# Kernel tuning notes

Hardware: AMD Instinct MI355X
Metric: run time of the kernel (lower is better)

Reference implementation:

```python
import jax, jax.numpy as jnp
import numpy as np

DILATIONS = [2 ** i for i in range(9)] * 3  # 27 layers
RD, SD, QD = 32, 512, 256


def conv1d(x, w, b, dilation=1, padding=0):
    # x: [B,C,T], w: [O,I,K], b: [O]
    out = jax.lax.conv_general_dilated(
        x, w, window_strides=(1,), padding=[(padding, padding)],
        rhs_dilation=(dilation,), dimension_numbers=('NCH', 'OIH', 'NCH'))
    return out + b[None, :, None]


def setup_inputs() -> dict:
    key = jax.random.key(0)
    ks = jax.random.split(key, 16)
    T = 131072
    L = len(DILATIONS)
    s = 0.05
    inp = {
        'x': jax.random.normal(ks[0], (1, 1, T), dtype=jnp.float32),
        'Wc': jax.random.normal(ks[1], (RD, 1, 3), dtype=jnp.float32) * s,
        'bc': jnp.zeros((RD,), dtype=jnp.float32),
        'Wt': jax.random.normal(ks[2], (L, RD, RD, 3), dtype=jnp.float32) * s,
        'bt': jnp.zeros((L, RD), dtype=jnp.float32),
        'Ws': jax.random.normal(ks[3], (L, RD, RD, 3), dtype=jnp.float32) * s,
        'bs': jnp.zeros((L, RD), dtype=jnp.float32),
        'Wskip': jax.random.normal(ks[4], (L, SD, RD, 1), dtype=jnp.float32) * s,
        'bskip': jnp.zeros((L, SD), dtype=jnp.float32),
        'Wdense': jax.random.normal(ks[5], (L, RD, RD, 1), dtype=jnp.float32) * s,
        'bdense': jnp.zeros((L, RD), dtype=jnp.float32),
        'Wp1': jax.random.normal(ks[6], (SD, SD, 1), dtype=jnp.float32) * s,
        'bp1': jnp.zeros((SD,), dtype=jnp.float32),
        'Wp2': jax.random.normal(ks[7], (QD, SD, 1), dtype=jnp.float32) * s,
        'bp2': jnp.zeros((QD,), dtype=jnp.float32),
    }
    return inp


def reference(x, Wc, bc, Wt, bt, Ws, bs, Wskip, bskip, Wdense, bdense, Wp1, bp1, Wp2, bp2):
    # causal conv: kernel 3, padding 1 (same length)
    x = conv1d(x, Wc, bc, dilation=1, padding=1)  # [1, RD, T]
    skip = jnp.zeros((1, SD, x.shape[2]), dtype=jnp.float32)
    for i, d in enumerate(DILATIONS):
        xin = x
        g = jnp.tanh(conv1d(x, Wt[i], bt[i], d, d)) * jax.nn.sigmoid(conv1d(x, Ws[i], bs[i], d, d))
        skip = skip + conv1d(g, Wskip[i], bskip[i])
        x = conv1d(g, Wdense[i], bdense[i]) + xin
    # NOTE: the original applies F.relu(x) on the residual path but then
    # overwrites x with the skip-path result, so that relu is dead code.
    out = conv1d(jax.nn.relu(conv1d(skip, Wp1, bp1)), Wp2, bp2)  # [1, QD, T]
    return jax.nn.log_softmax(out, axis=1)
```

## Files before the change

### kernel.cpp

```cpp
#include <hip/hip_runtime.h>

#define T_LEN 131072
#define RD 32
#define SD 512
#define QD 256
#define NL 27
#define KTOT (NL * RD)
#define GPAD 256

typedef __attribute__((ext_vector_type(8))) short short8;
typedef __attribute__((ext_vector_type(4))) float floatx4;

__device__ __forceinline__ unsigned short f2bf(float f) {
    union { float f; unsigned int i; } v; v.f = f;
    unsigned int r = v.i + 0x7fffu + ((v.i >> 16) & 1u);
    return (unsigned short)(r >> 16);
}

__device__ __forceinline__ void gload_lds16(const void* g, void* l) {
    __builtin_amdgcn_global_load_lds(
        (const __attribute__((address_space(1))) unsigned int*)g,
        (__attribute__((address_space(3))) unsigned int*)l, 16, 0, 0);
}

__global__ __launch_bounds__(256)
void k_conv_init(const float* __restrict__ x, const float* __restrict__ Wc,
                 const float* __restrict__ bc,
                 float* __restrict__ xaG, unsigned short* __restrict__ xabG,
                 float* __restrict__ xbG, unsigned short* __restrict__ xbbG)
{
    const int gid = blockIdx.x * 256 + threadIdx.x;

    if (gid < 4 * GPAD * RD) {
        const int region = gid >> 13;
        const int idx = gid & (GPAD * RD - 1);
        float* fg; unsigned short* hg;
        const size_t post = (size_t)(GPAD + T_LEN) * RD;
        switch (region) {
            case 0:  fg = xaG;        hg = xabG;        break;
            case 1:  fg = xaG + post; hg = xabG + post; break;
            case 2:  fg = xbG;        hg = xbbG;        break;
            default: fg = xbG + post; hg = xbbG + post; break;
        }
        fg[idx] = 0.f;
        hg[idx] = 0;
    }

    const int t = gid;
    const float xm = (t > 0) ? x[t - 1] : 0.f;
    const float x0 = x[t];
    const float xp = (t < T_LEN - 1) ? x[t + 1] : 0.f;
    float* row = xaG + (size_t)(GPAD + t) * RD;
    unsigned short* rowb = xabG + (size_t)(GPAD + t) * RD;
#pragma unroll
    for (int o = 0; o < RD; ++o) {
        const float v = bc[o] + Wc[o * 3 + 0] * xm + Wc[o * 3 + 1] * x0 + Wc[o * 3 + 2] * xp;
        row[o] = v;
        rowb[o] = f2bf(v);
    }
}

__global__ __launch_bounds__(256)
void k_wprep(const float* __restrict__ Wt, const float* __restrict__ Ws,
             const float* __restrict__ Wd,
             unsigned short* __restrict__ Wg, unsigned short* __restrict__ Wdb)
{
    const int idx = blockIdx.x * 256 + threadIdx.x;
    const int n1 = NL * 64 * 96;
    const int n2 = NL * RD * RD;
    if (idx < n1) {
        const int l = idx / (64 * 96);
        const int rem = idx % (64 * 96);
        const int m = rem / 96;
        const int k = rem % 96;
        const int j = k / 32;
        const int c = k % 32;
        float v;
        if (m < 32) v = Wt[(((size_t)l * RD + m) * RD + c) * 3 + j];
        else        v = Ws[(((size_t)l * RD + (m - 32)) * RD + c) * 3 + j];
        Wg[idx] = f2bf(v);
    } else if (idx < n1 + n2) {
        const int i2 = idx - n1;
        Wdb[i2] = f2bf(Wd[i2]);
    }
}

__global__ __launch_bounds__(256, 4)
void k_layer_stage(const float* __restrict__ xin,
                   const unsigned short* __restrict__ xinb,
                   float* __restrict__ xout,
                   unsigned short* __restrict__ xoutb,
                   unsigned short* __restrict__ Gt,
                   const unsigned short* __restrict__ Wg,
                   const unsigned short* __restrict__ Wdb,
                   const float* __restrict__ bt, const float* __restrict__ bs,
                   const float* __restrict__ bd, int d, int layer)
{
    __shared__ unsigned short bandsL[3][128 * 32];
    __shared__ unsigned short gtileL[128 * 32];

    const int tid = threadIdx.x;
    const int lane = tid & 63;
    const int w = tid >> 6;
    const int quad = lane >> 4;
    const int l16 = lane & 15;
    const int rbase = w * 32;
    const bool last = (layer == NL - 1);
    const floatx4 vzero = {0.f, 0.f, 0.f, 0.f};

    const int r16c = lane >> 2;
    const int scB = (lane & 3) ^ ((lane >> 3) & 3);
    const long long gbase = (long long)blockIdx.x * 128 + rbase;

#pragma unroll
    for (int j = 0; j < 3; ++j) {
        const long long b0 = gbase + (long long)(j - 1) * d;
#pragma unroll
        for (int i = 0; i < 2; ++i)
            gload_lds16(xinb + (b0 + i * 16 + r16c) * RD + scB * 8,
                        &bandsL[j][(rbase + i * 16) * 32]);
    }
    asm volatile("" ::: "memory");

    floatx4 xi[2][2];
    if (!last) {
#pragma unroll
        for (int nt = 0; nt < 2; ++nt) {
            const long long t = gbase + nt * 16 + l16;
#pragma unroll
            for (int mt = 0; mt < 2; ++mt)
                xi[nt][mt] = *reinterpret_cast<const floatx4*>(
                    xin + (size_t)t * RD + mt * 16 + quad * 4);
        }
    }
    asm volatile("s_waitcnt vmcnt(8)" ::: "memory");

    short8 afr[3][4];
#pragma unroll
    for (int j = 0; j < 3; ++j)
#pragma unroll
        for (int mt = 0; mt < 4; ++mt)
            afr[j][mt] = *reinterpret_cast<const short8*>(
                Wg + (size_t)(mt * 16 + l16) * 96 + j * 32 + quad * 8);

    floatx4 acc[4][2];
#pragma unroll
    for (int mt = 0; mt < 4; ++mt)
#pragma unroll
        for (int nt = 0; nt < 2; ++nt) acc[mt][nt] = vzero;

#pragma unroll
    for (int nt = 0; nt < 2; ++nt) {
        const int rloc = rbase + nt * 16 + l16;
        const int key2 = (rloc >> 1) & 3;
#pragma unroll
        for (int j = 0; j < 3; ++j) {
            const short8 bb = *reinterpret_cast<const short8*>(
                &bandsL[j][rloc * 32 + ((quad ^ key2) * 8)]);
#pragma unroll
            for (int mt = 0; mt < 4; ++mt)
                acc[mt][nt] = __builtin_amdgcn_mfma_f32_16x16x32_bf16(
                    afr[j][mt], bb, acc[mt][nt], 0, 0, 0);
        }
    }

#pragma unroll
    for (int nt = 0; nt < 2; ++nt) {
        const int rloc = rbase + nt * 16 + l16;
        const int key2 = (rloc >> 1) & 3;
        const long long t = (long long)blockIdx.x * 128 + rloc;
#pragma unroll
        for (int pair = 0; pair < 2; ++pair) {
            const floatx4 bt4 = *reinterpret_cast<const floatx4*>(bt + pair * 16 + quad * 4);
            const floatx4 bs4 = *reinterpret_cast<const floatx4*>(bs + pair * 16 + quad * 4);
            ushort4 u;
            unsigned short us[4];
#pragma unroll
            for (int r = 0; r < 4; ++r) {
                const float a1 = acc[pair][nt][r] + bt4[r];
                const float a2 = acc[2 + pair][nt][r] + bs4[r];
                const float th = 1.f - __fdividef(2.f, __expf(2.f * a1) + 1.f);
                const float sg = __fdividef(1.f, 1.f + __expf(-a2));
                us[r] = f2bf(th * sg);
            }
            u.x = us[0]; u.y = us[1]; u.z = us[2]; u.w = us[3];
            const int cbase = pair * 16 + quad * 4;
            if (!last) {
                const int colS = (pair * 2 + (quad >> 1)) ^ key2;
                *reinterpret_cast<ushort4*>(
                    &gtileL[rloc * 32 + colS * 8 + (quad & 1) * 4]) = u;
            }
            *reinterpret_cast<ushort4*>(
                Gt + ((size_t)layer * T_LEN + t) * RD + cbase) = u;
        }
    }

    if (!last) {
        short8 ad[2];
#pragma unroll
        for (int mt = 0; mt < 2; ++mt)
            ad[mt] = *reinterpret_cast<const short8*>(
                Wdb + (size_t)(mt * 16 + l16) * RD + quad * 8);

#pragma unroll
        for (int nt = 0; nt < 2; ++nt) {
            const int rloc = rbase + nt * 16 + l16;
            const int key2 = (rloc >> 1) & 3;
            const long long t = (long long)blockIdx.x * 128 + rloc;
            const short8 bg = *reinterpret_cast<const short8*>(
                &gtileL[rloc * 32 + ((quad ^ key2) * 8)]);
#pragma unroll
            for (int mt = 0; mt < 2; ++mt) {
                const floatx4 a2v = __builtin_amdgcn_mfma_f32_16x16x32_bf16(
                    ad[mt], bg, vzero, 0, 0, 0);
                const int m = mt * 16 + quad * 4;
                const floatx4 bd4 = *reinterpret_cast<const floatx4*>(bd + m);
                floatx4 o;
                ushort4 ob;
                o[0] = a2v[0] + bd4[0] + xi[nt][mt][0]; ob.x = f2bf(o[0]);
                o[1] = a2v[1] + bd4[1] + xi[nt][mt][1]; ob.y = f2bf(o[1]);
                o[2] = a2v[2] + bd4[2] + xi[nt][mt][2]; ob.z = f2bf(o[2]);
                o[3] = a2v[3] + bd4[3] + xi[nt][mt][3]; ob.w = f2bf(o[3]);
                *reinterpret_cast<floatx4*>(xout + (size_t)t * RD + m) = o;
                *reinterpret_cast<ushort4*>(xoutb + (size_t)t * RD + m) = ob;
            }
        }
    }
}

__global__ __launch_bounds__(256)
void k_wcomb(const float* __restrict__ Wp1, const float* __restrict__ Wskip,
             unsigned short* __restrict__ Wcomb)
{
    const int idx = blockIdx.x * 256 + threadIdx.x;
    if (idx >= SD * KTOT) return;
    const int m = idx / KTOT;
    const int k = idx % KTOT;
    const int l = k / RD;
    const int c = k % RD;
    const float* wp1r = Wp1 + (size_t)m * SD;
    const float* wsk = Wskip + (size_t)l * SD * RD + c;
    float acc = 0.f;
    for (int j = 0; j < SD; ++j) acc += wp1r[j] * wsk[(size_t)j * RD];
    Wcomb[((size_t)l * SD + m) * RD + c] = f2bf(acc);
}

__global__ __launch_bounds__(512)
void k_hbias(const float* __restrict__ Wp1, const float* __restrict__ bp1,
             const float* __restrict__ bskip, float* __restrict__ hbias)
{
    __shared__ float sb[SD];
    const int tid = threadIdx.x;
    float s = 0.f;
    for (int l = 0; l < NL; ++l) s += bskip[l * SD + tid];
    sb[tid] = s;
    __syncthreads();
    float acc = bp1[tid];
    const float* r = Wp1 + (size_t)tid * SD;
    for (int j = 0; j < SD; ++j) acc += r[j] * sb[j];
    hbias[tid] = acc;
}

__global__ __launch_bounds__(256)
void k_cvt(const float* __restrict__ src, unsigned short* __restrict__ dst, int n)
{
    const int i = blockIdx.x * 256 + threadIdx.x;
    if (i < n) dst[i] = f2bf(src[i]);
}

__global__ __launch_bounds__(256)
void k_gemm1(const unsigned short* __restrict__ A,
             const unsigned short* __restrict__ B,
             const float* __restrict__ hbias,
             unsigned short* __restrict__ ht)
{
    __shared__ unsigned short ldsA[2][128 * 32];
    __shared__ unsigned short ldsB[2][128 * 32];
    const int tid = threadIdx.x;
    const int lane = tid & 63;
    const int w = tid >> 6;
    const int wm = w & 1;
    const int wn = w >> 1;
    const int quad = lane >> 4;
    const int l16 = lane & 15;

    const int g = blockIdx.x;
    const int m0 = ((g >> 3) & 3) * 128;
    const int n0 = ((g & 7) + 8 * (g >> 5)) * 128;

    const int r4 = lane >> 2;
    const int c4 = lane & 3;
    const int srcc = c4 ^ ((r4 >> 1) & 3);
    const int swz = (l16 >> 1) & 3;

    floatx4 acc[4][4];
    const floatx4 vzero = {0.f, 0.f, 0.f, 0.f};
#pragma unroll
    for (int mt = 0; mt < 4; ++mt)
#pragma unroll
        for (int nt = 0; nt < 4; ++nt) acc[mt][nt] = vzero;

    const unsigned short* pA = A + (size_t)(m0 + r4) * RD + srcc * 8;
    const unsigned short* pB = B + (size_t)(n0 + r4) * RD + srcc * 8;

    for (int kc2 = 0; kc2 < 13; ++kc2) {
#pragma unroll
        for (int s = 0; s < 2; ++s) {
            const int kc = kc2 * 2 + s;
#pragma unroll
            for (int c = 0; c < 2; ++c) {
                const int row = w * 32 + c * 16;
                gload_lds16(pA + ((size_t)kc * SD + row) * RD, &ldsA[s][row * 32]);
                gload_lds16(pB + ((size_t)kc * T_LEN + row) * RD, &ldsB[s][row * 32]);
            }
        }
        __syncthreads();

#pragma unroll
        for (int s = 0; s < 2; ++s) {
            short8 afr[4], bfr[4];
#pragma unroll
            for (int mt = 0; mt < 4; ++mt)
                afr[mt] = *reinterpret_cast<const short8*>(
                    &ldsA[s][(wm * 64 + mt * 16 + l16) * 32 + (quad ^ swz) * 8]);
#pragma unroll
            for (int nt = 0; nt < 4; ++nt)
                bfr[nt] = *reinterpret_cast<const short8*>(
                    &ldsB[s][(wn * 64 + nt * 16 + l16) * 32 + (quad ^ swz) * 8]);
#pragma unroll
            for (int mt = 0; mt < 4; ++mt)
#pragma unroll
                for (int nt = 0; nt < 4; ++nt)
                    acc[mt][nt] = __builtin_amdgcn_mfma_f32_16x16x32_bf16(
                        afr[mt], bfr[nt], acc[mt][nt], 0, 0, 0);
        }
        __syncthreads();
    }
    {
        const int kc = 26;
#pragma unroll
        for (int c = 0; c < 2; ++c) {
            const int row = w * 32 + c * 16;
            gload_lds16(pA + ((size_t)kc * SD + row) * RD, &ldsA[0][row * 32]);
            gload_lds16(pB + ((size_t)kc * T_LEN + row) * RD, &ldsB[0][row * 32]);
        }
        __syncthreads();
        short8 afr[4], bfr[4];
#pragma unroll
        for (int mt = 0; mt < 4; ++mt)
            afr[mt] = *reinterpret_cast<const short8*>(
                &ldsA[0][(wm * 64 + mt * 16 + l16) * 32 + (quad ^ swz) * 8]);
#pragma unroll
        for (int nt = 0; nt < 4; ++nt)
            bfr[nt] = *reinterpret_cast<const short8*>(
                &ldsB[0][(wn * 64 + nt * 16 + l16) * 32 + (quad ^ swz) * 8]);
#pragma unroll
        for (int mt = 0; mt < 4; ++mt)
#pragma unroll
            for (int nt = 0; nt < 4; ++nt)
                acc[mt][nt] = __builtin_amdgcn_mfma_f32_16x16x32_bf16(
                    afr[mt], bfr[nt], acc[mt][nt], 0, 0, 0);
    }

#pragma unroll
    for (int mt = 0; mt < 4; ++mt) {
        const int m = m0 + wm * 64 + mt * 16 + quad * 4;
        const floatx4 hb = *reinterpret_cast<const floatx4*>(hbias + m);
        const size_t chunkbase = (size_t)(m >> 5) * T_LEN;
        const int mc = m & 31;
#pragma unroll
        for (int nt = 0; nt < 4; ++nt) {
            const int t = n0 + wn * 64 + nt * 16 + l16;
            ushort4 st;
            float v;
            v = acc[mt][nt][0] + hb[0]; st.x = f2bf(v > 0.f ? v : 0.f);
            v = acc[mt][nt][1] + hb[1]; st.y = f2bf(v > 0.f ? v : 0.f);
            v = acc[mt][nt][2] + hb[2]; st.z = f2bf(v > 0.f ? v : 0.f);
            v = acc[mt][nt][3] + hb[3]; st.w = f2bf(v > 0.f ? v : 0.f);
            *reinterpret_cast<ushort4*>(ht + (chunkbase + t) * RD + mc) = st;
        }
    }
}

__global__ __launch_bounds__(256)
void k_gemm2_lsm(const unsigned short* __restrict__ A,
                 const unsigned short* __restrict__ B,
                 const float* __restrict__ bp2,
                 float* __restrict__ out)
{
    __shared__ unsigned short ldsB[4][64 * 32];
    __shared__ float redmax[4 * 16 * 16];
    __shared__ float redsum[4 * 16 * 16];
    const int tid = threadIdx.x;
    const int lane = tid & 63;
    const int w = tid >> 6;
    const int quad = lane >> 4;
    const int l16 = lane & 15;
    const int m0 = w * 64;
    const int n0 = blockIdx.x * 64;

    const int r4 = lane >> 2;
    const int c4 = lane & 3;
    const int srcc = c4 ^ ((r4 >> 1) & 3);
    const int swz = (l16 >> 1) & 3;

    const unsigned short* ab[4];
#pragma unroll
    for (int mt = 0; mt < 4; ++mt)
        ab[mt] = A + (size_t)(m0 + mt * 16 + l16) * SD + quad * 8;

    const unsigned short* pB = B + (size_t)(n0 + w * 16 + r4) * RD + srcc * 8;

    floatx4 acc[4][4];
    const floatx4 vzero = {0.f, 0.f, 0.f, 0.f};
#pragma unroll
    for (int mt = 0; mt < 4; ++mt)
#pragma unroll
        for (int nt = 0; nt < 4; ++nt) acc[mt][nt] = vzero;

    for (int kc4 = 0; kc4 < 4; ++kc4) {
#pragma unroll
        for (int s = 0; s < 4; ++s)
            gload_lds16(pB + (size_t)(kc4 * 4 + s) * T_LEN * RD,
                        &ldsB[s][(w * 16) * 32]);
        __syncthreads();

#pragma unroll
        for (int s = 0; s < 4; ++s) {
            const int kc = kc4 * 4 + s;
            short8 afr[4];
#pragma unroll
            for (int mt = 0; mt < 4; ++mt)
                afr[mt] = *reinterpret_cast<const short8*>(ab[mt] + kc * 32);
            short8 bfr[4];
#pragma unroll
            for (int nt = 0; nt < 4; ++nt)
                bfr[nt] = *reinterpret_cast<const short8*>(
                    &ldsB[s][(nt * 16 + l16) * 32 + (quad ^ swz) * 8]);
#pragma unroll
            for (int mt = 0; mt < 4; ++mt)
#pragma unroll
                for (int nt = 0; nt < 4; ++nt)
                    acc[mt][nt] = __builtin_amdgcn_mfma_f32_16x16x32_bf16(
                        afr[mt], bfr[nt], acc[mt][nt], 0, 0, 0);
        }
        __syncthreads();
    }

#pragma unroll
    for (int mt = 0; mt < 4; ++mt) {
        const int mb = m0 + mt * 16 + quad * 4;
        const floatx4 bz = *reinterpret_cast<const floatx4*>(bp2 + mb);
#pragma unroll
        for (int nt = 0; nt < 4; ++nt)
#pragma unroll
            for (int j = 0; j < 4; ++j) acc[mt][nt][j] += bz[j];
    }

#pragma unroll
    for (int nt = 0; nt < 4; ++nt) {
        float lm = -1e30f;
#pragma unroll
        for (int mt = 0; mt < 4; ++mt)
#pragma unroll
            for (int j = 0; j < 4; ++j) lm = fmaxf(lm, acc[mt][nt][j]);
        redmax[nt * 256 + l16 * 16 + w * 4 + quad] = lm;
    }
    __syncthreads();

    float lse[4];
#pragma unroll
    for (int nt = 0; nt < 4; ++nt) {
        float gm = -1e30f;
#pragma unroll
        for (int i = 0; i < 16; ++i) gm = fmaxf(gm, redmax[nt * 256 + l16 * 16 + i]);
        float ls = 0.f;
#pragma unroll
        for (int mt = 0; mt < 4; ++mt)
#pragma unroll
            for (int j = 0; j < 4; ++j) ls += __expf(acc[mt][nt][j] - gm);
        redsum[nt * 256 + l16 * 16 + w * 4 + quad] = ls;
        lse[nt] = gm;
    }
    __syncthreads();

#pragma unroll
    for (int nt = 0; nt < 4; ++nt) {
        float tot = 0.f;
#pragma unroll
        for (int i = 0; i < 16; ++i) tot += redsum[nt * 256 + l16 * 16 + i];
        lse[nt] = lse[nt] + __logf(tot);
    }

#pragma unroll
    for (int mt = 0; mt < 4; ++mt) {
        const int mb = m0 + mt * 16 + quad * 4;
#pragma unroll
        for (int nt = 0; nt < 4; ++nt) {
            const int t = n0 + nt * 16 + l16;
#pragma unroll
            for (int j = 0; j < 4; ++j)
                out[(size_t)(mb + j) * T_LEN + t] = acc[mt][nt][j] - lse[nt];
        }
    }
}

extern "C" void kernel_launch(void* const* d_in, const int* in_sizes, int n_in,
                              void* d_out, int out_size, void* d_ws, size_t ws_size,
                              hipStream_t stream)
{
    (void)in_sizes; (void)n_in; (void)out_size; (void)ws_size;
    const float* x     = (const float*)d_in[0];
    const float* Wc    = (const float*)d_in[1];
    const float* bc    = (const float*)d_in[2];
    const float* Wt    = (const float*)d_in[3];
    const float* bt    = (const float*)d_in[4];
    const float* Ws    = (const float*)d_in[5];
    const float* bs    = (const float*)d_in[6];
    const float* Wskip = (const float*)d_in[7];
    const float* bskip = (const float*)d_in[8];
    const float* Wd    = (const float*)d_in[9];
    const float* bd    = (const float*)d_in[10];
    const float* Wp1   = (const float*)d_in[11];
    const float* bp1   = (const float*)d_in[12];
    const float* Wp2   = (const float*)d_in[13];
    const float* bp2   = (const float*)d_in[14];
    float* out = (float*)d_out;

    char* p = (char*)d_ws;
    unsigned short* Gt = (unsigned short*)p;    p += (size_t)T_LEN * KTOT * 2;
    unsigned short* ht = (unsigned short*)p;    p += (size_t)T_LEN * SD * 2;
    unsigned short* Wcomb = (unsigned short*)p; p += (size_t)SD * KTOT * 2;
    unsigned short* Wp2b = (unsigned short*)p;  p += (size_t)QD * SD * 2;
    unsigned short* Wg = (unsigned short*)p;    p += (size_t)NL * 64 * 96 * 2;
    unsigned short* Wdb = (unsigned short*)p;   p += (size_t)NL * RD * RD * 2;
    float* hbias = (float*)p;                   p += (size_t)SD * 4;

    char* q = (char*)ht;
    const size_t grows = (size_t)(T_LEN + 2 * GPAD) * RD;
    float* xaG = (float*)q;                     q += grows * 4;
    float* xbG = (float*)q;                     q += grows * 4;
    unsigned short* xabG = (unsigned short*)q;  q += grows * 2;
    unsigned short* xbbG = (unsigned short*)q;  q += grows * 2;
    float* xa = xaG + (size_t)GPAD * RD;
    float* xb = xbG + (size_t)GPAD * RD;
    unsigned short* xab = xabG + (size_t)GPAD * RD;
    unsigned short* xbb = xbbG + (size_t)GPAD * RD;

    k_wcomb<<<(SD * KTOT + 255) / 256, 256, 0, stream>>>(Wp1, Wskip, Wcomb);
    k_hbias<<<1, 512, 0, stream>>>(Wp1, bp1, bskip, hbias);
    k_cvt<<<(QD * SD + 255) / 256, 256, 0, stream>>>(Wp2, Wp2b, QD * SD);
    {
        const int nprep = NL * 64 * 96 + NL * RD * RD;
        k_wprep<<<(nprep + 255) / 256, 256, 0, stream>>>(Wt, Ws, Wd, Wg, Wdb);
    }
    k_conv_init<<<T_LEN / 256, 256, 0, stream>>>(x, Wc, bc, xaG, xabG, xbG, xbbG);

    static const int dil[NL] = {1, 2, 4, 8, 16, 32, 64, 128, 256,
                                1, 2, 4, 8, 16, 32, 64, 128, 256,
                                1, 2, 4, 8, 16, 32, 64, 128, 256};
    const float* cur = xa;
    const unsigned short* curb = xab;
    float* nxt = xb;
    unsigned short* nxtb = xbb;
    for (int i = 0; i < NL; ++i) {
        k_layer_stage<<<T_LEN / 128, 256, 0, stream>>>(
            cur, curb, nxt, nxtb, Gt,
            Wg + (size_t)i * 64 * 96,
            Wdb + (size_t)i * RD * RD,
            bt + (size_t)i * RD,
            bs + (size_t)i * RD,
            bd + (size_t)i * RD,
            dil[i], i);
        { float* tf = (float*)cur; cur = nxt; nxt = tf; }
        { unsigned short* tb = (unsigned short*)curb; curb = nxtb; nxtb = tb; }
    }

    k_gemm1<<<4 * (T_LEN / 128), 256, 0, stream>>>(Wcomb, Gt, hbias, ht);
    k_gemm2_lsm<<<T_LEN / 64, 256, 0, stream>>>(Wp2b, ht, bp2, out);
}
```

Before: 926.9 us.

## Store residual stream as bf16 hi/lo split instead of fp32 plus bf16 copy

```diff
diff --git a/kernel.cpp b/kernel.cpp
--- a/kernel.cpp
+++ b/kernel.cpp
@@ -17,6 +17,11 @@
     return (unsigned short)(r >> 16);
 }
 
+__device__ __forceinline__ float bf2f(unsigned short h) {
+    union { unsigned int i; float f; } u; u.i = (unsigned int)h << 16;
+    return u.f;
+}
+
 __device__ __forceinline__ void gload_lds16(const void* g, void* l) {
     __builtin_amdgcn_global_load_lds(
         (const __attribute__((address_space(1))) unsigned int*)g,
@@ -26,23 +31,22 @@
 __global__ __launch_bounds__(256)
 void k_conv_init(const float* __restrict__ x, const float* __restrict__ Wc,
                  const float* __restrict__ bc,
-                 float* __restrict__ xaG, unsigned short* __restrict__ xabG,
-                 float* __restrict__ xbG, unsigned short* __restrict__ xbbG)
+                 unsigned short* __restrict__ xahG, unsigned short* __restrict__ xalG,
+                 unsigned short* __restrict__ xbhG)
 {
     const int gid = blockIdx.x * 256 + threadIdx.x;
 
     if (gid < 4 * GPAD * RD) {
         const int region = gid >> 13;
         const int idx = gid & (GPAD * RD - 1);
-        float* fg; unsigned short* hg;
+        unsigned short* hg;
         const size_t post = (size_t)(GPAD + T_LEN) * RD;
         switch (region) {
-            case 0:  fg = xaG;        hg = xabG;        break;
-            case 1:  fg = xaG + post; hg = xabG + post; break;
-            case 2:  fg = xbG;        hg = xbbG;        break;
-            default: fg = xbG + post; hg = xbbG + post; break;
-        }
-        fg[idx] = 0.f;
+            case 0:  hg = xahG;        break;
+            case 1:  hg = xahG + post; break;
+            case 2:  hg = xbhG;        break;
+            default: hg = xbhG + post; break;
+        }
         hg[idx] = 0;
     }
 
@@ -50,13 +54,14 @@
     const float xm = (t > 0) ? x[t - 1] : 0.f;
     const float x0 = x[t];
     const float xp = (t < T_LEN - 1) ? x[t + 1] : 0.f;
-    float* row = xaG + (size_t)(GPAD + t) * RD;
-    unsigned short* rowb = xabG + (size_t)(GPAD + t) * RD;
+    unsigned short* rowh = xahG + (size_t)(GPAD + t) * RD;
+    unsigned short* rowl = xalG + (size_t)(GPAD + t) * RD;
 #pragma unroll
     for (int o = 0; o < RD; ++o) {
         const float v = bc[o] + Wc[o * 3 + 0] * xm + Wc[o * 3 + 1] * x0 + Wc[o * 3 + 2] * xp;
-        row[o] = v;
-        rowb[o] = f2bf(v);
+        const unsigned short h = f2bf(v);
+        rowh[o] = h;
+        rowl[o] = f2bf(v - bf2f(h));
     }
 }
 
@@ -86,10 +91,10 @@
 }
 
 __global__ __launch_bounds__(256, 4)
-void k_layer_stage(const float* __restrict__ xin,
-                   const unsigned short* __restrict__ xinb,
-                   float* __restrict__ xout,
-                   unsigned short* __restrict__ xoutb,
+void k_layer_stage(const unsigned short* __restrict__ xinh,
+                   const unsigned short* __restrict__ xinl,
+                   unsigned short* __restrict__ xouth,
+                   unsigned short* __restrict__ xoutl,
                    unsigned short* __restrict__ Gt,
                    const unsigned short* __restrict__ Wg,
                    const unsigned short* __restrict__ Wdb,
@@ -97,6 +102,7 @@
                    const float* __restrict__ bd, int d, int layer)
 {
     __shared__ unsigned short bandsL[3][128 * 32];
+    __shared__ unsigned short loL[128 * 32];
     __shared__ unsigned short gtileL[128 * 32];
 
     const int tid = threadIdx.x;
@@ -117,23 +123,20 @@
         const long long b0 = gbase + (long long)(j - 1) * d;
 #pragma unroll
         for (int i = 0; i < 2; ++i)
-            gload_lds16(xinb + (b0 + i * 16 + r16c) * RD + scB * 8,
+            gload_lds16(xinh + (b0 + i * 16 + r16c) * RD + scB * 8,
                         &bandsL[j][(rbase + i * 16) * 32]);
     }
     asm volatile("" ::: "memory");
 
-    floatx4 xi[2][2];
     if (!last) {
 #pragma unroll
-        for (int nt = 0; nt < 2; ++nt) {
-            const long long t = gbase + nt * 16 + l16;
-#pragma unroll
-            for (int mt = 0; mt < 2; ++mt)
-                xi[nt][mt] = *reinterpret_cast<const floatx4*>(
-                    xin + (size_t)t * RD + mt * 16 + quad * 4);
-        }
-    }
-    asm volatile("s_waitcnt vmcnt(8)" ::: "memory");
+        for (int i = 0; i < 2; ++i)
+            gload_lds16(xinl + (gbase + i * 16 + r16c) * RD + scB * 8,
+                        &loL[(rbase + i * 16) * 32]);
+        asm volatile("s_waitcnt vmcnt(2)" ::: "memory");
+    } else {
+        asm volatile("s_waitcnt vmcnt(0)" ::: "memory");
+    }
 
     short8 afr[3][4];
 #pragma unroll
@@ -163,6 +166,8 @@
                     afr[j][mt], bb, acc[mt][nt], 0, 0, 0);
         }
     }
+
+    if (!last) asm volatile("s_waitcnt vmcnt(0)" ::: "memory");
 
 #pragma unroll
     for (int nt = 0; nt < 2; ++nt) {
@@ -214,15 +219,22 @@
                 const floatx4 a2v = __builtin_amdgcn_mfma_f32_16x16x32_bf16(
                     ad[mt], bg, vzero, 0, 0, 0);
                 const int m = mt * 16 + quad * 4;
+                const int colS2 = (mt * 2 + (quad >> 1)) ^ key2;
+                const int off = rloc * 32 + colS2 * 8 + (quad & 1) * 4;
+                const ushort4 hi4 = *reinterpret_cast<const ushort4*>(&bandsL[1][off]);
+                const ushort4 lo4 = *reinterpret_cast<const ushort4*>(&loL[off]);
                 const floatx4 bd4 = *reinterpret_cast<const floatx4*>(bd + m);
-                floatx4 o;
-                ushort4 ob;
-                o[0] = a2v[0] + bd4[0] + xi[nt][mt][0]; ob.x = f2bf(o[0]);
-                o[1] = a2v[1] + bd4[1] + xi[nt][mt][1]; ob.y = f2bf(o[1]);
-                o[2] = a2v[2] + bd4[2] + xi[nt][mt][2]; ob.z = f2bf(o[2]);
-                o[3] = a2v[3] + bd4[3] + xi[nt][mt][3]; ob.w = f2bf(o[3]);
-                *reinterpret_cast<floatx4*>(xout + (size_t)t * RD + m) = o;
-                *reinterpret_cast<ushort4*>(xoutb + (size_t)t * RD + m) = ob;
+                float o0 = a2v[0] + bd4[0] + bf2f(hi4.x) + bf2f(lo4.x);
+                float o1 = a2v[1] + bd4[1] + bf2f(hi4.y) + bf2f(lo4.y);
+                float o2 = a2v[2] + bd4[2] + bf2f(hi4.z) + bf2f(lo4.z);
+                float o3 = a2v[3] + bd4[3] + bf2f(hi4.w) + bf2f(lo4.w);
+                ushort4 oh, ol;
+                oh.x = f2bf(o0); ol.x = f2bf(o0 - bf2f(oh.x));
+                oh.y = f2bf(o1); ol.y = f2bf(o1 - bf2f(oh.y));
+                oh.z = f2bf(o2); ol.z = f2bf(o2 - bf2f(oh.z));
+                oh.w = f2bf(o3); ol.w = f2bf(o3 - bf2f(oh.w));
+                *reinterpret_cast<ushort4*>(xouth + (size_t)t * RD + m) = oh;
+                *reinterpret_cast<ushort4*>(xoutl + (size_t)t * RD + m) = ol;
             }
         }
     }
@@ -538,14 +550,14 @@
 
     char* q = (char*)ht;
     const size_t grows = (size_t)(T_LEN + 2 * GPAD) * RD;
-    float* xaG = (float*)q;                     q += grows * 4;
-    float* xbG = (float*)q;                     q += grows * 4;
-    unsigned short* xabG = (unsigned short*)q;  q += grows * 2;
-    unsigned short* xbbG = (unsigned short*)q;  q += grows * 2;
-    float* xa = xaG + (size_t)GPAD * RD;
-    float* xb = xbG + (size_t)GPAD * RD;
-    unsigned short* xab = xabG + (size_t)GPAD * RD;
-    unsigned short* xbb = xbbG + (size_t)GPAD * RD;
+    unsigned short* xahG = (unsigned short*)q;  q += grows * 2;
+    unsigned short* xalG = (unsigned short*)q;  q += grows * 2;
+    unsigned short* xbhG = (unsigned short*)q;  q += grows * 2;
+    unsigned short* xblG = (unsigned short*)q;  q += grows * 2;
+    unsigned short* xah = xahG + (size_t)GPAD * RD;
+    unsigned short* xal = xalG + (size_t)GPAD * RD;
+    unsigned short* xbh = xbhG + (size_t)GPAD * RD;
+    unsigned short* xbl = xblG + (size_t)GPAD * RD;
 
     k_wcomb<<<(SD * KTOT + 255) / 256, 256, 0, stream>>>(Wp1, Wskip, Wcomb);
     k_hbias<<<1, 512, 0, stream>>>(Wp1, bp1, bskip, hbias);
@@ -554,26 +566,26 @@
         const int nprep = NL * 64 * 96 + NL * RD * RD;
         k_wprep<<<(nprep + 255) / 256, 256, 0, stream>>>(Wt, Ws, Wd, Wg, Wdb);
     }
-    k_conv_init<<<T_LEN / 256, 256, 0, stream>>>(x, Wc, bc, xaG, xabG, xbG, xbbG);
+    k_conv_init<<<T_LEN / 256, 256, 0, stream>>>(x, Wc, bc, xahG, xalG, xbhG);
 
     static const int dil[NL] = {1, 2, 4, 8, 16, 32, 64, 128, 256,
                                 1, 2, 4, 8, 16, 32, 64, 128, 256,
                                 1, 2, 4, 8, 16, 32, 64, 128, 256};
-    const float* cur = xa;
-    const unsigned short* curb = xab;
-    float* nxt = xb;
-    unsigned short* nxtb = xbb;
+    const unsigned short* curh = xah;
+    const unsigned short* curl = xal;
+    unsigned short* nxth = xbh;
+    unsigned short* nxtl = xbl;
     for (int i = 0; i < NL; ++i) {
         k_layer_stage<<<T_LEN / 128, 256, 0, stream>>>(
-            cur, curb, nxt, nxtb, Gt,
+            curh, curl, nxth, nxtl, Gt,
             Wg + (size_t)i * 64 * 96,
             Wdb + (size_t)i * RD * RD,
             bt + (size_t)i * RD,
             bs + (size_t)i * RD,
             bd + (size_t)i * RD,
             dil[i], i);
-        { float* tf = (float*)cur; cur = nxt; nxt = tf; }
-        { unsigned short* tb = (unsigned short*)curb; curb = nxtb; nxtb = tb; }
+        { unsigned short* th = (unsigned short*)curh; curh = nxth; nxth = th; }
+        { unsigned short* tl = (unsigned short*)curl; curl = nxtl; nxtl = tl; }
     }
 
     k_gemm1<<<4 * (T_LEN / 128), 256, 0, stream>>>(Wcomb, Gt, hbias, ht);
```

New measurement: 894.9 us (median of 2 runs). 3.4% less time.
